# Optimization experiments

Measured on AMD Instinct MI355X. Metric: run time of the kernel, lower is better.

The kernel has to match this reference:

```python
import jax, jax.numpy as jnp
import numpy as np

B, S, H = 1, 2048, 2048
I = 1408
E = 64
TOP_K = 8
N_GROUP = 8
TOPK_GROUP = 4
SCALE = 2.5
N_SHARED = 2


def setup_inputs() -> dict:
    key = jax.random.key(0)
    ks = jax.random.split(key, 9)
    x = jax.random.normal(ks[0], (B, S, H), dtype=jnp.float32)
    # kaiming_uniform(a=sqrt(5)) for [E, H] weight -> bound = 1/sqrt(H)
    gate_w = jax.random.uniform(ks[1], (E, H), jnp.float32, -1.0, 1.0) / jnp.sqrt(float(H))
    e_bias = jnp.zeros((E,), jnp.float32)
    gate_proj = jax.random.normal(ks[2], (E, I, H), jnp.float32) * 0.02
    up_proj = jax.random.normal(ks[3], (E, I, H), jnp.float32) * 0.02
    down_proj = jax.random.normal(ks[4], (E, H, I), jnp.float32) * 0.02
    SI = I * N_SHARED
    shared_gate_w = jax.random.uniform(ks[5], (SI, H), jnp.float32, -1.0, 1.0) / jnp.sqrt(float(H))
    shared_up_w = jax.random.uniform(ks[6], (SI, H), jnp.float32, -1.0, 1.0) / jnp.sqrt(float(H))
    shared_down_w = jax.random.uniform(ks[7], (H, SI), jnp.float32, -1.0, 1.0) / jnp.sqrt(float(SI))
    return {"hidden_states": x, "gate_w": gate_w, "e_bias": e_bias,
            "gate_proj": gate_proj, "up_proj": up_proj, "down_proj": down_proj,
            "shared_gate_w": shared_gate_w, "shared_up_w": shared_up_w,
            "shared_down_w": shared_down_w}


def _moe_forward(hidden_states, gate_w, e_bias, gate_proj, up_proj, down_proj,
                 shared_gate_w, shared_up_w, shared_down_w):
    bsz, seq_len, h = hidden_states.shape
    xf = hidden_states.reshape(-1, h).astype(jnp.float32)  # [T, H]
    T = bsz * seq_len

    # ---- DeepSeek group-restricted top-k gating ----
    logits = xf @ gate_w.T                                  # [T, E]
    scores = jax.nn.sigmoid(logits)
    scores_for_choice = scores + e_bias[None, :]
    gs = scores_for_choice.reshape(T, N_GROUP, E // N_GROUP)
    group_scores = jax.lax.top_k(gs, 2)[0].sum(-1)          # [T, n_group] sum of top-2 per group
    group_idx = jax.lax.top_k(group_scores, TOPK_GROUP)[1]  # [T, topk_group]
    group_mask = jax.nn.one_hot(group_idx, N_GROUP, dtype=jnp.float32).sum(1)  # [T, n_group]
    score_mask = jnp.repeat(group_mask, E // N_GROUP, axis=1)                  # [T, E]
    tmp_scores = jnp.where(score_mask > 0, scores_for_choice, 0.0)
    topk_idx = jax.lax.top_k(tmp_scores, TOP_K)[1]          # [T, top_k]
    topk_w = jnp.take_along_axis(scores, topk_idx, axis=1)  # gather from UN-biased scores
    topk_w = topk_w / (topk_w.sum(-1, keepdims=True) + 1e-20)
    topk_w = topk_w * SCALE

    # Dense combine weights [T, E]; exactly equivalent to sort/dispatch/combine.
    rows = jnp.arange(T)
    cw = jnp.zeros((T, E), jnp.float32).at[rows[:, None], topk_idx].add(topk_w)

    # ---- per-expert FFN, accumulated with lax.scan over the (fixed) expert axis ----
    def step(y, we):
        Wg, Wu, Wd, w = we                                  # [I,H],[I,H],[H,I],[T]
        g = xf @ Wg.T                                       # [T, I]
        u = xf @ Wu.T
        inter = jax.nn.silu(g) * u                          # silu_mul kernel
        out = inter @ Wd.T                                  # [T, H]
        return y + out * w[:, None], None

    y0 = jnp.zeros_like(xf)
    y, _ = jax.lax.scan(step, y0, (gate_proj, up_proj, down_proj, cw.T))
    y = y.reshape(bsz, seq_len, h)

    # ---- shared experts ----
    sg = hidden_states @ shared_gate_w.T                    # [B, S, SI]
    su = hidden_states @ shared_up_w.T
    shared_out = (jax.nn.silu(sg) * su) @ shared_down_w.T   # [B, S, H]
    return y + shared_out


def reference(hidden_states, gate_w, e_bias, gate_proj, up_proj, down_proj,
              shared_gate_w, shared_up_w, shared_down_w):
    return _moe_forward(hidden_states, gate_w, e_bias, gate_proj, up_proj, down_proj,
                        shared_gate_w, shared_up_w, shared_down_w)
```

## Files before the change

### kernel.cpp

```cpp
#include <hip/hip_runtime.h>

typedef unsigned short u16;
typedef unsigned int u32;
typedef __attribute__((ext_vector_type(8))) short short8;
typedef __attribute__((ext_vector_type(8))) u16 ushort8;
typedef __attribute__((ext_vector_type(4))) float f32x4;
typedef __attribute__((ext_vector_type(4))) u32 u32x4;

#define T_TOK 2048
#define H_DIM 2048
#define NEXP 64
#define I_DIM 1408
#define SI_DIM 2816
#define BM 128
#define BK 64
#define MAXT 512

__device__ __forceinline__ u16 f2bf(float f) {
    u32 u = __builtin_bit_cast(u32, f);
    u32 r = u + 0x7FFFu + ((u >> 16) & 1u);
    return (u16)(r >> 16);
}

__device__ __forceinline__ float bf2f(u16 v) {
    u32 u = ((u32)v) << 16;
    return __builtin_bit_cast(float, u);
}

__device__ __forceinline__ u32 cvtpk(float lo, float hi) {
    u32 r;
    asm("v_cvt_pk_bf16_f32 %0, %1, %2" : "=v"(r) : "v"(lo), "v"(hi));
    return r;
}

__device__ __forceinline__ ushort8 cvt8(f32x4 a, f32x4 b) {
    u32x4 p;
    p[0] = cvtpk(a[0], a[1]);
    p[1] = cvtpk(a[2], a[3]);
    p[2] = cvtpk(b[0], b[1]);
    p[3] = cvtpk(b[2], b[3]);
    return __builtin_bit_cast(ushort8, p);
}

__device__ __forceinline__ f32x4 mfma16(short8 a, short8 b, f32x4 c) {
    return __builtin_amdgcn_mfma_f32_16x16x32_bf16(a, b, c, 0, 0, 0);
}

__device__ __forceinline__ void gld_lds16(const void* g, void* l) {
    __builtin_amdgcn_global_load_lds(
        (const __attribute__((address_space(1))) void*)(g),
        (__attribute__((address_space(3))) void*)(l), 16, 0, 0);
}

__global__ __launch_bounds__(256) void k_cvt(const float* __restrict__ x, u16* __restrict__ xb) {
    int i = (blockIdx.x * 256 + threadIdx.x) * 8;
    f32x4 v0 = *(const f32x4*)(x + i);
    f32x4 v1 = *(const f32x4*)(x + i + 4);
    *(ushort8*)(xb + i) = cvt8(v0, v1);
}

__global__ __launch_bounds__(256) void k_gate_logits(const float* __restrict__ x,
        const float* __restrict__ gw, float* __restrict__ logits) {
    __shared__ float xs[8][65];
    __shared__ float wsh[64][65];
    int tid = threadIdx.x;
    int t0 = blockIdx.x * 8;
    double acc0 = 0.0, acc1 = 0.0;
    int e = tid & 63, tg = tid >> 6;
    for (int k0 = 0; k0 < H_DIM; k0 += 64) {
        #pragma unroll
        for (int s = 0; s < 2; ++s) {
            int idx = s * 256 + tid;
            int r = idx >> 6, k = idx & 63;
            xs[r][k] = x[(size_t)(t0 + r) * H_DIM + k0 + k];
        }
        #pragma unroll
        for (int s = 0; s < 16; ++s) {
            int idx = s * 256 + tid;
            int r = idx >> 6, k = idx & 63;
            wsh[r][k] = gw[(size_t)r * H_DIM + k0 + k];
        }
        __syncthreads();
        #pragma unroll 8
        for (int k = 0; k < 64; ++k) {
            double wv = (double)wsh[e][k];
            acc0 += (double)xs[tg][k] * wv;
            acc1 += (double)xs[tg + 4][k] * wv;
        }
        __syncthreads();
    }
    logits[(size_t)(t0 + tg) * NEXP + e] = (float)acc0;
    logits[(size_t)(t0 + tg + 4) * NEXP + e] = (float)acc1;
}

__global__ __launch_bounds__(256) void k_topk(const float* __restrict__ logits,
        const float* __restrict__ ebias, int* __restrict__ topk_idx,
        float* __restrict__ topk_w, int* __restrict__ counts) {
    __shared__ float bsh[64];
    if (threadIdx.x < 64) bsh[threadIdx.x] = ebias[threadIdx.x];
    __syncthreads();
    int t = blockIdx.x * 256 + threadIdx.x;
    float sc[64];
    #pragma unroll
    for (int e2 = 0; e2 < 64; ++e2) {
        float lg = logits[(size_t)t * 64 + e2];
        sc[e2] = 1.0f / (1.0f + expf(-lg));
    }
    float gsc[8];
    #pragma unroll
    for (int g = 0; g < 8; ++g) {
        float m1 = -1e30f, m2 = -1e30f;
        #pragma unroll
        for (int j = 0; j < 8; ++j) {
            float v = sc[g * 8 + j] + bsh[g * 8 + j];
            if (v > m1) { m2 = m1; m1 = v; }
            else if (v > m2) { m2 = v; }
        }
        gsc[g] = m1 + m2;
    }
    u32 gmask = 0;
    #pragma unroll
    for (int it = 0; it < 4; ++it) {
        float best = -1e30f; int bi = 0;
        #pragma unroll
        for (int g = 0; g < 8; ++g) {
            bool ok = !((gmask >> g) & 1u);
            if (ok && gsc[g] > best) { best = gsc[g]; bi = g; }
        }
        gmask |= 1u << bi;
    }
    unsigned long long avail = 0ull;
    #pragma unroll
    for (int g = 0; g < 8; ++g)
        if ((gmask >> g) & 1u) avail |= (0xFFull << (g * 8));
    float wsum = 0.f;
    int idx[8]; float wv[8];
    #pragma unroll
    for (int it = 0; it < 8; ++it) {
        float best = -1e30f, bw = 0.f; int bi = 0;
        #pragma unroll
        for (int e2 = 0; e2 < 64; ++e2) {
            bool ok = (avail >> e2) & 1ull;
            float v = sc[e2] + bsh[e2];
            if (ok && v > best) { best = v; bi = e2; bw = sc[e2]; }
        }
        avail &= ~(1ull << bi);
        idx[it] = bi; wv[it] = bw; wsum += bw;
    }
    float scale = 2.5f / (wsum + 1e-20f);
    #pragma unroll
    for (int it = 0; it < 8; ++it) {
        topk_idx[t * 8 + it] = idx[it];
        topk_w[t * 8 + it] = wv[it] * scale;
        atomicAdd(&counts[idx[it]], 1);
    }
}

__global__ void k_prefix(const int* __restrict__ counts, int* __restrict__ offsets,
                         int* __restrict__ tiles_gu, int* __restrict__ tiles_dn) {
    if (threadIdx.x == 0) {
        int run = 0;
        for (int e = 0; e < 64; ++e) { offsets[e] = run; run += counts[e]; }
        offsets[64] = run;
        for (int i = 0; i < MAXT; ++i) { tiles_gu[i] = -1; tiles_dn[i] = -1; }
        int sg[8] = {0,0,0,0,0,0,0,0};
        int sd[8] = {0,0,0,0,0,0,0,0};
        for (int j = 0; j < SI_DIM / 64; ++j) {
            int xcd = j & 7;
            int pos = xcd + 8 * sg[xcd];
            if (pos < MAXT) { tiles_gu[pos] = (64 << 16) | (j * 64); sg[xcd]++; }
        }
        for (int j = 0; j < H_DIM / 128; ++j) {
            int xcd = j & 7;
            int pos = xcd + 8 * sd[xcd];
            if (pos < MAXT) { tiles_dn[pos] = (64 << 16) | (j * 128); sd[xcd]++; }
        }
        for (int e = 0; e < 64; ++e) {
            int xcd = e & 7;
            int c = counts[e];
            for (int m0 = 0; m0 < c; m0 += BM) {
                int pg = xcd + 8 * sg[xcd];
                if (pg < MAXT) { tiles_gu[pg] = (e << 16) | m0; sg[xcd]++; }
                int pd = xcd + 8 * sd[xcd];
                if (pd < MAXT) { tiles_dn[pd] = (e << 16) | m0; sd[xcd]++; }
            }
        }
    }
}

__global__ __launch_bounds__(256) void k_scatter(const int* __restrict__ topk_idx,
        const float* __restrict__ topk_w, const int* __restrict__ offsets,
        int* __restrict__ fill, int* __restrict__ tok_list, float* __restrict__ w_list,
        int* __restrict__ slot_of) {
    int gid = blockIdx.x * 256 + threadIdx.x;
    int t = gid >> 3;
    int e = topk_idx[gid];
    int pos = offsets[e] + atomicAdd(&fill[e], 1);
    tok_list[pos] = t;
    w_list[pos] = topk_w[gid];
    slot_of[gid] = pos;
}

__global__ __launch_bounds__(256, 2) void k_gateup(
        const u16* __restrict__ xb,
        const float* __restrict__ gr, const float* __restrict__ ur,
        const float* __restrict__ gs, const float* __restrict__ us,
        const int* __restrict__ offsets, const int* __restrict__ tok_list,
        const int* __restrict__ tiles,
        u16* __restrict__ inter_r, u16* __restrict__ inter_s) {
    int tt = tiles[blockIdx.x];
    if (tt < 0) return;
    int e = tt >> 16;
    const float *Bg, *Bu; u16* op; const int* tl;
    int m0, seg, n, i0, Irows;
    if (e < 64) {
        m0 = tt & 0xFFFF; seg = offsets[e]; n = offsets[e + 1] - seg;
        if (n <= 0 || m0 >= n) return;
        i0 = blockIdx.y * 64;
        Bg = gr + (size_t)e * I_DIM * H_DIM;
        Bu = ur + (size_t)e * I_DIM * H_DIM;
        op = inter_r; Irows = I_DIM; tl = tok_list;
    } else {
        if (blockIdx.y >= T_TOK / BM) return;
        i0 = tt & 0xFFFF; m0 = blockIdx.y * BM; seg = 0; n = T_TOK;
        Bg = gs; Bu = us;
        op = inter_s; Irows = SI_DIM; tl = nullptr;
    }

    __shared__ u16 As[2][BM * BK];
    __shared__ u16 Bsg[2][64 * BK];
    __shared__ u16 Bsu[2][64 * BK];

    int tid = threadIdx.x;
    int w = tid >> 6, lane = tid & 63;

    const u16* agsrc[4];
    #pragma unroll
    for (int s = 0; s < 4; ++s) {
        int slot = s * 256 + tid;
        int r = slot >> 3, cb = slot & 7;
        int p = m0 + r; if (p >= n) p = n - 1;
        int tok = tl ? tl[seg + p] : p;
        agsrc[s] = xb + (size_t)tok * H_DIM + ((cb ^ (r & 7)) * 8);
    }
    auto gldA = [&](int t, int buf) {
        #pragma unroll
        for (int s = 0; s < 4; ++s)
            gld_lds16(agsrc[s] + t * BK, (u16*)As[buf] + s * 2048 + w * 512);
    };

    const float* bgsrc[2]; const float* busrc[2]; int bdst[2];
    #pragma unroll
    for (int s = 0; s < 2; ++s) {
        int slot = s * 256 + tid;
        int r = slot >> 3, cb = slot & 7;
        bgsrc[s] = Bg + (size_t)(i0 + r) * H_DIM + cb * 8;
        busrc[s] = Bu + (size_t)(i0 + r) * H_DIM + cb * 8;
        bdst[s] = r * BK + ((cb ^ (r & 7)) * 8);
    }

    f32x4 zero; zero[0] = 0.f; zero[1] = 0.f; zero[2] = 0.f; zero[3] = 0.f;
    f32x4 accg[2][4], accu[2][4];
    #pragma unroll
    for (int a = 0; a < 2; ++a)
        #pragma unroll
        for (int b = 0; b < 4; ++b) { accg[a][b] = zero; accu[a][b] = zero; }

    f32x4 stG0[2][2], stU0[2][2], stG1[2][2], stU1[2][2];

    auto ldB0 = [&](int t) {
        int k0 = t * BK;
        #pragma unroll
        for (int s = 0; s < 2; ++s) {
            stG0[s][0] = *(const f32x4*)(bgsrc[s] + k0);
            stG0[s][1] = *(const f32x4*)(bgsrc[s] + k0 + 4);
            stU0[s][0] = *(const f32x4*)(busrc[s] + k0);
            stU0[s][1] = *(const f32x4*)(busrc[s] + k0 + 4);
        }
    };
    auto ldB1 = [&](int t) {
        int k0 = t * BK;
        #pragma unroll
        for (int s = 0; s < 2; ++s) {
            stG1[s][0] = *(const f32x4*)(bgsrc[s] + k0);
            stG1[s][1] = *(const f32x4*)(bgsrc[s] + k0 + 4);
            stU1[s][0] = *(const f32x4*)(busrc[s] + k0);
            stU1[s][1] = *(const f32x4*)(busrc[s] + k0 + 4);
        }
    };
    auto dswB0 = [&]() {
        #pragma unroll
        for (int s = 0; s < 2; ++s) {
            *(ushort8*)(&Bsg[0][bdst[s]]) = cvt8(stG0[s][0], stG0[s][1]);
            *(ushort8*)(&Bsu[0][bdst[s]]) = cvt8(stU0[s][0], stU0[s][1]);
        }
    };
    auto dswB1 = [&]() {
        #pragma unroll
        for (int s = 0; s < 2; ++s) {
            *(ushort8*)(&Bsg[1][bdst[s]]) = cvt8(stG1[s][0], stG1[s][1]);
            *(ushort8*)(&Bsu[1][bdst[s]]) = cvt8(stU1[s][0], stU1[s][1]);
        }
    };
    auto mmaStep = [&](int buf) {
        #pragma unroll
        for (int ks = 0; ks < 2; ++ks) {
            short8 a[2];
            #pragma unroll
            for (int fm = 0; fm < 2; ++fm) {
                int row = w * 32 + fm * 16 + (lane & 15);
                int cb = ks * 4 + (lane >> 4);
                a[fm] = *(const short8*)(&As[buf][row * BK + ((cb ^ (row & 7)) * 8)]);
            }
            #pragma unroll
            for (int fn = 0; fn < 4; ++fn) {
                int brow = fn * 16 + (lane & 15);
                int cb = ks * 4 + (lane >> 4);
                int boff = brow * BK + ((cb ^ (brow & 7)) * 8);
                short8 bg = *(const short8*)(&Bsg[buf][boff]);
                short8 bu = *(const short8*)(&Bsu[buf][boff]);
                accg[0][fn] = mfma16(a[0], bg, accg[0][fn]);
                accg[1][fn] = mfma16(a[1], bg, accg[1][fn]);
                accu[0][fn] = mfma16(a[0], bu, accu[0][fn]);
                accu[1][fn] = mfma16(a[1], bu, accu[1][fn]);
            }
        }
    };

    const int NK = H_DIM / BK;
    gldA(0, 0);
    ldB0(0); dswB0();
    ldB1(1);
    __syncthreads();
    for (int t = 0; t < NK; t += 2) {
        if (t + 1 < NK) gldA(t + 1, 1);
        if (t + 2 < NK) ldB0(t + 2);
        mmaStep(0);
        if (t + 1 < NK) dswB1();
        __syncthreads();
        if (t + 1 < NK) {
            if (t + 2 < NK) gldA(t + 2, 0);
            if (t + 3 < NK) ldB1(t + 3);
            mmaStep(1);
            if (t + 2 < NK) dswB0();
            __syncthreads();
        }
    }

    int r0 = (lane >> 4) * 4, cc = lane & 15;
    #pragma unroll
    for (int fm = 0; fm < 2; ++fm) {
        #pragma unroll
        for (int r = 0; r < 4; ++r) {
            int p = m0 + w * 32 + fm * 16 + r0 + r;
            if (p < n) {
                size_t rowb = (size_t)(seg + p) * Irows + i0;
                #pragma unroll
                for (int fn = 0; fn < 4; ++fn) {
                    float g = accg[fm][fn][r], u = accu[fm][fn][r];
                    float val = g / (1.0f + expf(-g)) * u;
                    op[rowb + fn * 16 + cc] = f2bf(val);
                }
            }
        }
    }
}

__global__ __launch_bounds__(256, 2) void k_down(
        const u16* __restrict__ inter_r, const u16* __restrict__ inter_s,
        const float* __restrict__ dr, const float* __restrict__ dsw,
        const int* __restrict__ offsets, const int* __restrict__ tok_list,
        const int* __restrict__ tiles,
        const float* __restrict__ w_list,
        u16* __restrict__ y_r, float* __restrict__ out) {
    int tt = tiles[blockIdx.x];
    if (tt < 0) return;
    int e = tt >> 16;
    const float* Bd; const u16* interp; const float* wl;
    int m0, seg, n, h0, Kdim;
    if (e < 64) {
        m0 = tt & 0xFFFF; seg = offsets[e]; n = offsets[e + 1] - seg;
        if (n <= 0 || m0 >= n) return;
        h0 = blockIdx.y * 128;
        Bd = dr + (size_t)e * H_DIM * I_DIM;
        interp = inter_r; Kdim = I_DIM; wl = w_list;
    } else {
        h0 = tt & 0xFFFF; m0 = blockIdx.y * BM; seg = 0; n = T_TOK;
        Bd = dsw; interp = inter_s; Kdim = SI_DIM; wl = nullptr;
    }

    __shared__ u16 As[2][BM * BK];
    __shared__ u16 Bs[2][128 * BK];

    int tid = threadIdx.x;
    int w = tid >> 6, lane = tid & 63;

    const u16* agsrc[4];
    #pragma unroll
    for (int s = 0; s < 4; ++s) {
        int slot = s * 256 + tid;
        int r = slot >> 3, cb = slot & 7;
        int p = m0 + r; if (p >= n) p = n - 1;
        agsrc[s] = interp + (size_t)(seg + p) * Kdim + ((cb ^ (r & 7)) * 8);
    }
    auto gldA = [&](int t, int buf) {
        #pragma unroll
        for (int s = 0; s < 4; ++s)
            gld_lds16(agsrc[s] + t * BK, (u16*)As[buf] + s * 2048 + w * 512);
    };

    const float* bsrc[4]; int bdst[4];
    #pragma unroll
    for (int s = 0; s < 4; ++s) {
        int slot = s * 256 + tid;
        int r = slot >> 3, cb = slot & 7;
        bsrc[s] = Bd + (size_t)(h0 + r) * Kdim + cb * 8;
        bdst[s] = r * BK + ((cb ^ (r & 7)) * 8);
    }

    f32x4 zero; zero[0] = 0.f; zero[1] = 0.f; zero[2] = 0.f; zero[3] = 0.f;
    f32x4 acc[2][8];
    #pragma unroll
    for (int a = 0; a < 2; ++a)
        #pragma unroll
        for (int b = 0; b < 8; ++b) acc[a][b] = zero;

    f32x4 stB0[4][2], stB1[4][2];

    auto ldB0 = [&](int t) {
        int k0 = t * BK;
        #pragma unroll
        for (int s = 0; s < 4; ++s) {
            stB0[s][0] = *(const f32x4*)(bsrc[s] + k0);
            stB0[s][1] = *(const f32x4*)(bsrc[s] + k0 + 4);
        }
    };
    auto ldB1 = [&](int t) {
        int k0 = t * BK;
        #pragma unroll
        for (int s = 0; s < 4; ++s) {
            stB1[s][0] = *(const f32x4*)(bsrc[s] + k0);
            stB1[s][1] = *(const f32x4*)(bsrc[s] + k0 + 4);
        }
    };
    auto dswB0 = [&]() {
        #pragma unroll
        for (int s = 0; s < 4; ++s)
            *(ushort8*)(&Bs[0][bdst[s]]) = cvt8(stB0[s][0], stB0[s][1]);
    };
    auto dswB1 = [&]() {
        #pragma unroll
        for (int s = 0; s < 4; ++s)
            *(ushort8*)(&Bs[1][bdst[s]]) = cvt8(stB1[s][0], stB1[s][1]);
    };
    auto mmaStep = [&](int buf) {
        #pragma unroll
        for (int ks = 0; ks < 2; ++ks) {
            short8 a[2];
            #pragma unroll
            for (int fm = 0; fm < 2; ++fm) {
                int row = w * 32 + fm * 16 + (lane & 15);
                int cb = ks * 4 + (lane >> 4);
                a[fm] = *(const short8*)(&As[buf][row * BK + ((cb ^ (row & 7)) * 8)]);
            }
            #pragma unroll
            for (int fn = 0; fn < 8; ++fn) {
                int brow = fn * 16 + (lane & 15);
                int cb = ks * 4 + (lane >> 4);
                short8 b = *(const short8*)(&Bs[buf][brow * BK + ((cb ^ (brow & 7)) * 8)]);
                acc[0][fn] = mfma16(a[0], b, acc[0][fn]);
                acc[1][fn] = mfma16(a[1], b, acc[1][fn]);
            }
        }
    };

    const int NK = Kdim / BK;
    gldA(0, 0);
    ldB0(0); dswB0();
    ldB1(1);
    __syncthreads();
    for (int t = 0; t < NK; t += 2) {
        if (t + 1 < NK) gldA(t + 1, 1);
        if (t + 2 < NK) ldB0(t + 2);
        mmaStep(0);
        if (t + 1 < NK) dswB1();
        __syncthreads();
        if (t + 1 < NK) {
            if (t + 2 < NK) gldA(t + 2, 0);
            if (t + 3 < NK) ldB1(t + 3);
            mmaStep(1);
            if (t + 2 < NK) dswB0();
            __syncthreads();
        }
    }

    int r0 = (lane >> 4) * 4, cc = lane & 15;
    #pragma unroll
    for (int fm = 0; fm < 2; ++fm) {
        #pragma unroll
        for (int r = 0; r < 4; ++r) {
            int p = m0 + w * 32 + fm * 16 + r0 + r;
            if (p < n) {
                if (wl) {
                    float wt = wl[seg + p];
                    size_t ob = (size_t)(seg + p) * H_DIM + h0 + cc;
                    #pragma unroll
                    for (int fn = 0; fn < 8; ++fn)
                        y_r[ob + fn * 16] = f2bf(acc[fm][fn][r] * wt);
                } else {
                    size_t ob = (size_t)p * H_DIM + h0 + cc;
                    #pragma unroll
                    for (int fn = 0; fn < 8; ++fn)
                        out[ob + fn * 16] = acc[fm][fn][r];
                }
            }
        }
    }
}

__global__ __launch_bounds__(256) void k_combine(const u16* __restrict__ y_r,
        const int* __restrict__ slot_of, float* __restrict__ out) {
    int t = blockIdx.x;
    int c = threadIdx.x * 8;
    int sl[8];
    #pragma unroll
    for (int k = 0; k < 8; ++k) sl[k] = slot_of[t * 8 + k];
    float s[8];
    f32x4 o0 = *(const f32x4*)(out + (size_t)t * H_DIM + c);
    f32x4 o1 = *(const f32x4*)(out + (size_t)t * H_DIM + c + 4);
    #pragma unroll
    for (int j = 0; j < 4; ++j) { s[j] = o0[j]; s[4 + j] = o1[j]; }
    #pragma unroll
    for (int k = 0; k < 8; ++k) {
        ushort8 v = *(const ushort8*)(y_r + (size_t)sl[k] * H_DIM + c);
        #pragma unroll
        for (int j = 0; j < 8; ++j) s[j] += bf2f(v[j]);
    }
    f32x4 r0, r1;
    #pragma unroll
    for (int j = 0; j < 4; ++j) { r0[j] = s[j]; r1[j] = s[4 + j]; }
    *(f32x4*)(out + (size_t)t * H_DIM + c) = r0;
    *(f32x4*)(out + (size_t)t * H_DIM + c + 4) = r1;
}

extern "C" void kernel_launch(void* const* d_in, const int* in_sizes, int n_in,
                              void* d_out, int out_size, void* d_ws, size_t ws_size,
                              hipStream_t stream) {
    const float* x         = (const float*)d_in[0];
    const float* gate_w    = (const float*)d_in[1];
    const float* e_bias    = (const float*)d_in[2];
    const float* gate_proj = (const float*)d_in[3];
    const float* up_proj   = (const float*)d_in[4];
    const float* down_proj = (const float*)d_in[5];
    const float* sgw       = (const float*)d_in[6];
    const float* suw       = (const float*)d_in[7];
    const float* sdw       = (const float*)d_in[8];
    float* out = (float*)d_out;

    char* ws = (char*)d_ws;
    size_t off = 0;
    auto alloc = [&](size_t bytes) -> char* {
        char* p = ws + off;
        off += (bytes + 255) & ~(size_t)255;
        return p;
    };
    float* logits   = (float*)alloc((size_t)T_TOK * 64 * 4);
    int*   topk_idx = (int*)  alloc((size_t)T_TOK * 8 * 4);
    float* topk_w   = (float*)alloc((size_t)T_TOK * 8 * 4);
    int*   counts   = (int*)  alloc(256);
    int*   offsets  = (int*)  alloc(512);
    int*   fill     = (int*)  alloc(256);
    int*   tiles_gu = (int*)  alloc(MAXT * 4);
    int*   tiles_dn = (int*)  alloc(MAXT * 4);
    int*   tok_list = (int*)  alloc((size_t)T_TOK * 8 * 4);
    float* w_list   = (float*)alloc((size_t)T_TOK * 8 * 4);
    int*   slot_of  = (int*)  alloc((size_t)T_TOK * 8 * 4);
    u16*   xb       = (u16*)  alloc((size_t)T_TOK * H_DIM * 2);
    u16*   inter_r  = (u16*)  alloc((size_t)T_TOK * 8 * I_DIM * 2);
    u16*   inter_s  = (u16*)  alloc((size_t)T_TOK * SI_DIM * 2);
    u16*   y_r      = (u16*)  alloc((size_t)T_TOK * 8 * H_DIM * 2);

    hipMemsetAsync(counts, 0, 1024, stream);

    k_cvt<<<(T_TOK * H_DIM) / 2048, 256, 0, stream>>>(x, xb);
    k_gate_logits<<<T_TOK / 8, 256, 0, stream>>>(x, gate_w, logits);
    k_topk<<<T_TOK / 256, 256, 0, stream>>>(logits, e_bias, topk_idx, topk_w, counts);
    k_prefix<<<1, 64, 0, stream>>>(counts, offsets, tiles_gu, tiles_dn);
    k_scatter<<<(T_TOK * 8) / 256, 256, 0, stream>>>(topk_idx, topk_w, offsets, fill,
                                                     tok_list, w_list, slot_of);

    k_gateup<<<dim3(MAXT, I_DIM / 64), 256, 0, stream>>>(
        xb, gate_proj, up_proj, sgw, suw, offsets, tok_list, tiles_gu,
        inter_r, inter_s);
    k_down<<<dim3(MAXT, H_DIM / 128), 256, 0, stream>>>(
        inter_r, inter_s, down_proj, sdw, offsets, tok_list, tiles_dn,
        w_list, y_r, out);
    k_combine<<<T_TOK, 256, 0, stream>>>(y_r, slot_of, out);
}
```

Baseline: 1.260 ms.

## Split MMA steps into halves with raw barriers, partial waitcnt and setprio

```diff
diff --git a/kernel.cpp b/kernel.cpp
--- a/kernel.cpp
+++ b/kernel.cpp
@@ -15,6 +15,12 @@
 #define BM 128
 #define BK 64
 #define MAXT 512
+
+#define RAWBAR __builtin_amdgcn_s_barrier()
+#define PRIO1 __builtin_amdgcn_s_setprio(1)
+#define PRIO0 __builtin_amdgcn_s_setprio(0)
+#define WAIT_VM8_LGKM0 asm volatile("s_waitcnt vmcnt(8) lgkmcnt(0)" ::: "memory")
+#define WAIT_VM0_LGKM0 asm volatile("s_waitcnt vmcnt(0) lgkmcnt(0)" ::: "memory")
 
 __device__ __forceinline__ u16 f2bf(float f) {
     u32 u = __builtin_bit_cast(u32, f);
@@ -302,28 +308,25 @@
             *(ushort8*)(&Bsu[1][bdst[s]]) = cvt8(stU1[s][0], stU1[s][1]);
         }
     };
-    auto mmaStep = [&](int buf) {
-        #pragma unroll
-        for (int ks = 0; ks < 2; ++ks) {
-            short8 a[2];
-            #pragma unroll
-            for (int fm = 0; fm < 2; ++fm) {
-                int row = w * 32 + fm * 16 + (lane & 15);
-                int cb = ks * 4 + (lane >> 4);
-                a[fm] = *(const short8*)(&As[buf][row * BK + ((cb ^ (row & 7)) * 8)]);
-            }
-            #pragma unroll
-            for (int fn = 0; fn < 4; ++fn) {
-                int brow = fn * 16 + (lane & 15);
-                int cb = ks * 4 + (lane >> 4);
-                int boff = brow * BK + ((cb ^ (brow & 7)) * 8);
-                short8 bg = *(const short8*)(&Bsg[buf][boff]);
-                short8 bu = *(const short8*)(&Bsu[buf][boff]);
-                accg[0][fn] = mfma16(a[0], bg, accg[0][fn]);
-                accg[1][fn] = mfma16(a[1], bg, accg[1][fn]);
-                accu[0][fn] = mfma16(a[0], bu, accu[0][fn]);
-                accu[1][fn] = mfma16(a[1], bu, accu[1][fn]);
-            }
+    auto mmaHalf = [&](int buf, int ks) {
+        short8 a[2];
+        #pragma unroll
+        for (int fm = 0; fm < 2; ++fm) {
+            int row = w * 32 + fm * 16 + (lane & 15);
+            int cb = ks * 4 + (lane >> 4);
+            a[fm] = *(const short8*)(&As[buf][row * BK + ((cb ^ (row & 7)) * 8)]);
+        }
+        #pragma unroll
+        for (int fn = 0; fn < 4; ++fn) {
+            int brow = fn * 16 + (lane & 15);
+            int cb = ks * 4 + (lane >> 4);
+            int boff = brow * BK + ((cb ^ (brow & 7)) * 8);
+            short8 bg = *(const short8*)(&Bsg[buf][boff]);
+            short8 bu = *(const short8*)(&Bsu[buf][boff]);
+            accg[0][fn] = mfma16(a[0], bg, accg[0][fn]);
+            accg[1][fn] = mfma16(a[1], bg, accg[1][fn]);
+            accu[0][fn] = mfma16(a[0], bu, accu[0][fn]);
+            accu[1][fn] = mfma16(a[1], bu, accu[1][fn]);
         }
     };
 
@@ -334,16 +337,24 @@
     __syncthreads();
     for (int t = 0; t < NK; t += 2) {
         if (t + 1 < NK) gldA(t + 1, 1);
+        PRIO1; mmaHalf(0, 0); PRIO0;
+        RAWBAR;
         if (t + 2 < NK) ldB0(t + 2);
-        mmaStep(0);
+        PRIO1; mmaHalf(0, 1); PRIO0;
         if (t + 1 < NK) dswB1();
-        __syncthreads();
+        if (t + 2 < NK) { WAIT_VM8_LGKM0; } else { WAIT_VM0_LGKM0; }
+        RAWBAR;
         if (t + 1 < NK) {
             if (t + 2 < NK) gldA(t + 2, 0);
+            PRIO1; mmaHalf(1, 0); PRIO0;
+            RAWBAR;
             if (t + 3 < NK) ldB1(t + 3);
-            mmaStep(1);
-            if (t + 2 < NK) dswB0();
-            __syncthreads();
+            PRIO1; mmaHalf(1, 1); PRIO0;
+            if (t + 2 < NK) {
+                dswB0();
+                if (t + 3 < NK) { WAIT_VM8_LGKM0; } else { WAIT_VM0_LGKM0; }
+                RAWBAR;
+            }
         }
     }
 
@@ -453,24 +464,21 @@
         for (int s = 0; s < 4; ++s)
             *(ushort8*)(&Bs[1][bdst[s]]) = cvt8(stB1[s][0], stB1[s][1]);
     };
-    auto mmaStep = [&](int buf) {
-        #pragma unroll
-        for (int ks = 0; ks < 2; ++ks) {
-            short8 a[2];
-            #pragma unroll
-            for (int fm = 0; fm < 2; ++fm) {
-                int row = w * 32 + fm * 16 + (lane & 15);
-                int cb = ks * 4 + (lane >> 4);
-                a[fm] = *(const short8*)(&As[buf][row * BK + ((cb ^ (row & 7)) * 8)]);
-            }
-            #pragma unroll
-            for (int fn = 0; fn < 8; ++fn) {
-                int brow = fn * 16 + (lane & 15);
-                int cb = ks * 4 + (lane >> 4);
-                short8 b = *(const short8*)(&Bs[buf][brow * BK + ((cb ^ (brow & 7)) * 8)]);
-                acc[0][fn] = mfma16(a[0], b, acc[0][fn]);
-                acc[1][fn] = mfma16(a[1], b, acc[1][fn]);
-            }
+    auto mmaHalf = [&](int buf, int ks) {
+        short8 a[2];
+        #pragma unroll
+        for (int fm = 0; fm < 2; ++fm) {
+            int row = w * 32 + fm * 16 + (lane & 15);
+            int cb = ks * 4 + (lane >> 4);
+            a[fm] = *(const short8*)(&As[buf][row * BK + ((cb ^ (row & 7)) * 8)]);
+        }
+        #pragma unroll
+        for (int fn = 0; fn < 8; ++fn) {
+            int brow = fn * 16 + (lane & 15);
+            int cb = ks * 4 + (lane >> 4);
+            short8 b = *(const short8*)(&Bs[buf][brow * BK + ((cb ^ (brow & 7)) * 8)]);
+            acc[0][fn] = mfma16(a[0], b, acc[0][fn]);
+            acc[1][fn] = mfma16(a[1], b, acc[1][fn]);
         }
     };
 
@@ -481,16 +489,24 @@
     __syncthreads();
     for (int t = 0; t < NK; t += 2) {
         if (t + 1 < NK) gldA(t + 1, 1);
+        PRIO1; mmaHalf(0, 0); PRIO0;
+        RAWBAR;
         if (t + 2 < NK) ldB0(t + 2);
-        mmaStep(0);
+        PRIO1; mmaHalf(0, 1); PRIO0;
         if (t + 1 < NK) dswB1();
-        __syncthreads();
+        if (t + 2 < NK) { WAIT_VM8_LGKM0; } else { WAIT_VM0_LGKM0; }
+        RAWBAR;
         if (t + 1 < NK) {
             if (t + 2 < NK) gldA(t + 2, 0);
+            PRIO1; mmaHalf(1, 0); PRIO0;
+            RAWBAR;
             if (t + 3 < NK) ldB1(t + 3);
-            mmaStep(1);
-            if (t + 2 < NK) dswB0();
-            __syncthreads();
+            PRIO1; mmaHalf(1, 1); PRIO0;
+            if (t + 2 < NK) {
+                dswB0();
+                if (t + 3 < NK) { WAIT_VM8_LGKM0; } else { WAIT_VM0_LGKM0; }
+                RAWBAR;
+            }
         }
     }
 
```

Measured after the change: 1.262 ms. About the same (+0.1%).

## Load fp32 weight tiles as contiguous 512-byte bursts spanning two K-steps

Applied to the files above, without the earlier changes.

```diff
diff --git a/kernel.cpp b/kernel.cpp
--- a/kernel.cpp
+++ b/kernel.cpp
@@ -249,15 +249,14 @@
             gld_lds16(agsrc[s] + t * BK, (u16*)As[buf] + s * 2048 + w * 512);
     };
 
-    const float* bgsrc[2]; const float* busrc[2]; int bdst[2];
-    #pragma unroll
-    for (int s = 0; s < 2; ++s) {
-        int slot = s * 256 + tid;
-        int r = slot >> 3, cb = slot & 7;
-        bgsrc[s] = Bg + (size_t)(i0 + r) * H_DIM + cb * 8;
-        busrc[s] = Bu + (size_t)(i0 + r) * H_DIM + cb * 8;
-        bdst[s] = r * BK + ((cb ^ (r & 7)) * 8);
-    }
+    int br = tid >> 2, bq = tid & 3;
+    const float* bgsrc = Bg + (size_t)(i0 + br) * H_DIM + bq * 32;
+    const float* busrc = Bu + (size_t)(i0 + br) * H_DIM + bq * 32;
+    int bdst[4];
+    #pragma unroll
+    for (int j = 0; j < 4; ++j)
+        bdst[j] = br * BK + (((((bq & 1) * 4 + j)) ^ (br & 7)) * 8);
+    bool oddgrp = (bq >> 1) != 0;
 
     f32x4 zero; zero[0] = 0.f; zero[1] = 0.f; zero[2] = 0.f; zero[3] = 0.f;
     f32x4 accg[2][4], accu[2][4];
@@ -266,40 +265,31 @@
         #pragma unroll
         for (int b = 0; b < 4; ++b) { accg[a][b] = zero; accu[a][b] = zero; }
 
-    f32x4 stG0[2][2], stU0[2][2], stG1[2][2], stU1[2][2];
-
-    auto ldB0 = [&](int t) {
-        int k0 = t * BK;
-        #pragma unroll
-        for (int s = 0; s < 2; ++s) {
-            stG0[s][0] = *(const f32x4*)(bgsrc[s] + k0);
-            stG0[s][1] = *(const f32x4*)(bgsrc[s] + k0 + 4);
-            stU0[s][0] = *(const f32x4*)(busrc[s] + k0);
-            stU0[s][1] = *(const f32x4*)(busrc[s] + k0 + 4);
-        }
-    };
-    auto ldB1 = [&](int t) {
-        int k0 = t * BK;
-        #pragma unroll
-        for (int s = 0; s < 2; ++s) {
-            stG1[s][0] = *(const f32x4*)(bgsrc[s] + k0);
-            stG1[s][1] = *(const f32x4*)(bgsrc[s] + k0 + 4);
-            stU1[s][0] = *(const f32x4*)(busrc[s] + k0);
-            stU1[s][1] = *(const f32x4*)(busrc[s] + k0 + 4);
-        }
-    };
-    auto dswB0 = [&]() {
-        #pragma unroll
-        for (int s = 0; s < 2; ++s) {
-            *(ushort8*)(&Bsg[0][bdst[s]]) = cvt8(stG0[s][0], stG0[s][1]);
-            *(ushort8*)(&Bsu[0][bdst[s]]) = cvt8(stU0[s][0], stU0[s][1]);
-        }
-    };
-    auto dswB1 = [&]() {
-        #pragma unroll
-        for (int s = 0; s < 2; ++s) {
-            *(ushort8*)(&Bsg[1][bdst[s]]) = cvt8(stG1[s][0], stG1[s][1]);
-            *(ushort8*)(&Bsu[1][bdst[s]]) = cvt8(stU1[s][0], stU1[s][1]);
+    f32x4 bG[8], bU[8];
+    auto burst = [&](int C) {
+        int k0 = C * 128;
+        #pragma unroll
+        for (int j = 0; j < 8; ++j) {
+            bG[j] = *(const f32x4*)(bgsrc + k0 + j * 4);
+            bU[j] = *(const f32x4*)(busrc + k0 + j * 4);
+        }
+    };
+    auto dswE = [&]() {
+        if (!oddgrp) {
+            #pragma unroll
+            for (int j = 0; j < 4; ++j) {
+                *(ushort8*)(&Bsg[0][bdst[j]]) = cvt8(bG[2 * j], bG[2 * j + 1]);
+                *(ushort8*)(&Bsu[0][bdst[j]]) = cvt8(bU[2 * j], bU[2 * j + 1]);
+            }
+        }
+    };
+    auto dswO = [&]() {
+        if (oddgrp) {
+            #pragma unroll
+            for (int j = 0; j < 4; ++j) {
+                *(ushort8*)(&Bsg[1][bdst[j]]) = cvt8(bG[2 * j], bG[2 * j + 1]);
+                *(ushort8*)(&Bsu[1][bdst[j]]) = cvt8(bU[2 * j], bU[2 * j + 1]);
+            }
         }
     };
     auto mmaStep = [&](int buf) {
@@ -329,20 +319,19 @@
 
     const int NK = H_DIM / BK;
     gldA(0, 0);
-    ldB0(0); dswB0();
-    ldB1(1);
+    burst(0);
+    dswE(); dswO();
     __syncthreads();
     for (int t = 0; t < NK; t += 2) {
         if (t + 1 < NK) gldA(t + 1, 1);
-        if (t + 2 < NK) ldB0(t + 2);
+        if (t > 0) dswO();
+        if (t + 2 < NK) burst(t / 2 + 1);
         mmaStep(0);
-        if (t + 1 < NK) dswB1();
         __syncthreads();
         if (t + 1 < NK) {
             if (t + 2 < NK) gldA(t + 2, 0);
-            if (t + 3 < NK) ldB1(t + 3);
+            if (t + 2 < NK) dswE();
             mmaStep(1);
-            if (t + 2 < NK) dswB0();
             __syncthreads();
         }
     }
@@ -409,14 +398,13 @@
             gld_lds16(agsrc[s] + t * BK, (u16*)As[buf] + s * 2048 + w * 512);
     };
 
-    const float* bsrc[4]; int bdst[4];
-    #pragma unroll
-    for (int s = 0; s < 4; ++s) {
-        int slot = s * 256 + tid;
-        int r = slot >> 3, cb = slot & 7;
-        bsrc[s] = Bd + (size_t)(h0 + r) * Kdim + cb * 8;
-        bdst[s] = r * BK + ((cb ^ (r & 7)) * 8);
-    }
+    int br = tid >> 1, bq = tid & 1;
+    const float* bsrc = Bd + (size_t)(h0 + br) * Kdim + bq * 64;
+    int bdst[8];
+    #pragma unroll
+    for (int m = 0; m < 8; ++m)
+        bdst[m] = br * BK + ((m ^ (br & 7)) * 8);
+    bool oddgrp = bq != 0;
 
     f32x4 zero; zero[0] = 0.f; zero[1] = 0.f; zero[2] = 0.f; zero[3] = 0.f;
     f32x4 acc[2][8];
@@ -425,33 +413,26 @@
         #pragma unroll
         for (int b = 0; b < 8; ++b) acc[a][b] = zero;
 
-    f32x4 stB0[4][2], stB1[4][2];
-
-    auto ldB0 = [&](int t) {
-        int k0 = t * BK;
-        #pragma unroll
-        for (int s = 0; s < 4; ++s) {
-            stB0[s][0] = *(const f32x4*)(bsrc[s] + k0);
-            stB0[s][1] = *(const f32x4*)(bsrc[s] + k0 + 4);
-        }
-    };
-    auto ldB1 = [&](int t) {
-        int k0 = t * BK;
-        #pragma unroll
-        for (int s = 0; s < 4; ++s) {
-            stB1[s][0] = *(const f32x4*)(bsrc[s] + k0);
-            stB1[s][1] = *(const f32x4*)(bsrc[s] + k0 + 4);
-        }
-    };
-    auto dswB0 = [&]() {
-        #pragma unroll
-        for (int s = 0; s < 4; ++s)
-            *(ushort8*)(&Bs[0][bdst[s]]) = cvt8(stB0[s][0], stB0[s][1]);
-    };
-    auto dswB1 = [&]() {
-        #pragma unroll
-        for (int s = 0; s < 4; ++s)
-            *(ushort8*)(&Bs[1][bdst[s]]) = cvt8(stB1[s][0], stB1[s][1]);
+    f32x4 bB[16];
+    auto burst = [&](int C) {
+        int k0 = C * 128;
+        #pragma unroll
+        for (int j = 0; j < 16; ++j)
+            bB[j] = *(const f32x4*)(bsrc + k0 + j * 4);
+    };
+    auto dswE = [&]() {
+        if (!oddgrp) {
+            #pragma unroll
+            for (int m = 0; m < 8; ++m)
+                *(ushort8*)(&Bs[0][bdst[m]]) = cvt8(bB[2 * m], bB[2 * m + 1]);
+        }
+    };
+    auto dswO = [&]() {
+        if (oddgrp) {
+            #pragma unroll
+            for (int m = 0; m < 8; ++m)
+                *(ushort8*)(&Bs[1][bdst[m]]) = cvt8(bB[2 * m], bB[2 * m + 1]);
+        }
     };
     auto mmaStep = [&](int buf) {
         #pragma unroll
@@ -476,20 +457,19 @@
 
     const int NK = Kdim / BK;
     gldA(0, 0);
-    ldB0(0); dswB0();
-    ldB1(1);
+    burst(0);
+    dswE(); dswO();
     __syncthreads();
     for (int t = 0; t < NK; t += 2) {
         if (t + 1 < NK) gldA(t + 1, 1);
-        if (t + 2 < NK) ldB0(t + 2);
+        if (t > 0) dswO();
+        if (t + 2 < NK) burst(t / 2 + 1);
         mmaStep(0);
-        if (t + 1 < NK) dswB1();
         __syncthreads();
         if (t + 1 < NK) {
             if (t + 2 < NK) gldA(t + 2, 0);
-            if (t + 3 < NK) ldB1(t + 3);
+            if (t + 2 < NK) dswE();
             mmaStep(1);
-            if (t + 2 < NK) dswB0();
             __syncthreads();
         }
     }
```

Measured after the change: 1.763 ms. 39.8% more time.
